# Kernel optimization log

Measured on AMD Instinct MI355X. Metric: run time of the kernel, lower is better.

The kernel has to match this reference:

```python
import jax, jax.numpy as jnp
import numpy as np

N = 50000      # num nodes
EG = 1600000   # num edges (avg degree 32)
IN = 64        # in_dim
OUT = 64       # out_dim
H = 4          # num_heads
D = OUT // H   # per-head dim


def setup_inputs() -> dict:
    key = jax.random.key(0)
    ks = jax.random.split(key, 12)
    s = 1.0 / np.sqrt(IN)
    return {
        "x": jax.random.normal(ks[0], (N, IN), jnp.float32),
        "edge_attr": jax.random.normal(ks[1], (EG, IN), jnp.float32),
        "edge_index": jax.random.randint(ks[2], (2, EG), 0, N, jnp.int32),
        "Wq": jax.random.uniform(ks[3], (OUT, IN), jnp.float32, -s, s),
        "bq": jax.random.uniform(ks[4], (OUT,), jnp.float32, -s, s),
        "Wk": jax.random.uniform(ks[5], (OUT, IN), jnp.float32, -s, s),
        "bk": jax.random.uniform(ks[6], (OUT,), jnp.float32, -s, s),
        "We": jax.random.uniform(ks[7], (OUT, IN), jnp.float32, -s, s),
        "be": jax.random.uniform(ks[8], (OUT,), jnp.float32, -s, s),
        "Wv": jax.random.uniform(ks[9], (OUT, IN), jnp.float32, -s, s),
        "bv": jax.random.uniform(ks[10], (OUT,), jnp.float32, -s, s),
    }


def reference(x, edge_attr, edge_index, Wq, bq, Wk, bk, We, be, Wv, bv):
    n = x.shape[0]
    # linear projections, reshaped to [*, H, D]
    Qh = (x @ Wq.T + bq).reshape(n, H, D)
    Kh = (x @ Wk.T + bk).reshape(n, H, D)
    Vh = (x @ Wv.T + bv).reshape(n, H, D)
    Ee = (edge_attr @ We.T + be).reshape(-1, H, D)
    src = edge_index[0]
    dst = edge_index[1]
    # per-edge score: sum_d K[src] * Q[dst] / sqrt(D) * E  -> [E, H]
    score = ((Kh[src] * Qh[dst]) * (1.0 / np.sqrt(D)) * Ee).sum(-1)
    score = jnp.exp(jnp.clip(score, -5.0, 5.0))            # [E, H]
    msg = Vh[src] * score[..., None]                        # [E, H, D]
    wV = jax.ops.segment_sum(msg, dst, num_segments=n)      # [N, H, D]
    # note: original forward returns wV without dividing by Z
    return wV.reshape(n, H * D)
```

## Files before the change

### kernel.cpp

```cpp
#include <hip/hip_runtime.h>


__global__ __launch_bounds__(256) void proj_kernel(
    const float* __restrict__ x,
    const float* __restrict__ Wq, const float* __restrict__ bq,
    const float* __restrict__ Wk, const float* __restrict__ bk,
    const float* __restrict__ Wv, const float* __restrict__ bv,
    float* __restrict__ Q, float* __restrict__ K, float* __restrict__ V,
    int n)
{
    __shared__ float WqT[64 * 65];
    __shared__ float WkT[64 * 65];
    __shared__ float WvT[64 * 65];
    __shared__ float xs[4][4][64];

    const int tid  = threadIdx.x;
    const int wave = tid >> 6;
    const int lane = tid & 63;

    #pragma unroll
    for (int k = 0; k < 16; ++k) {
        int idx = tid + k * 256;
        int j = idx >> 6, i = idx & 63;
        WqT[i * 65 + j] = Wq[idx];
        WkT[i * 65 + j] = Wk[idx];
        WvT[i * 65 + j] = Wv[idx];
    }
    const float bqv = bq[lane];
    const float bkv = bk[lane];
    const float bvv = bv[lane];
    __syncthreads();

    for (int blockbase = blockIdx.x * 16; blockbase < n;
         blockbase += gridDim.x * 16) {
        int base = blockbase + wave * 4;
        #pragma unroll
        for (int j = 0; j < 4; ++j) {
            int node = base + j;
            xs[wave][j][lane] = (node < n) ? x[node * 64 + lane] : 0.f;
        }
        __syncthreads();

        float accq[4], acck[4], accv[4];
        #pragma unroll
        for (int j = 0; j < 4; ++j) { accq[j] = bqv; acck[j] = bkv; accv[j] = bvv; }

        #pragma unroll
        for (int f = 0; f < 16; ++f) {
            float wq[4], wk[4], wv[4];
            #pragma unroll
            for (int u = 0; u < 4; ++u) {
                int i = 4 * f + u;
                wq[u] = WqT[i * 65 + lane];
                wk[u] = WkT[i * 65 + lane];
                wv[u] = WvT[i * 65 + lane];
            }
            #pragma unroll
            for (int j = 0; j < 4; ++j) {
                float4 xv = *reinterpret_cast<const float4*>(&xs[wave][j][4 * f]);
                accq[j] = fmaf(xv.x, wq[0], accq[j]);
                accq[j] = fmaf(xv.y, wq[1], accq[j]);
                accq[j] = fmaf(xv.z, wq[2], accq[j]);
                accq[j] = fmaf(xv.w, wq[3], accq[j]);
                acck[j] = fmaf(xv.x, wk[0], acck[j]);
                acck[j] = fmaf(xv.y, wk[1], acck[j]);
                acck[j] = fmaf(xv.z, wk[2], acck[j]);
                acck[j] = fmaf(xv.w, wk[3], acck[j]);
                accv[j] = fmaf(xv.x, wv[0], accv[j]);
                accv[j] = fmaf(xv.y, wv[1], accv[j]);
                accv[j] = fmaf(xv.z, wv[2], accv[j]);
                accv[j] = fmaf(xv.w, wv[3], accv[j]);
            }
        }

        #pragma unroll
        for (int j = 0; j < 4; ++j) {
            int node = base + j;
            if (node < n) {
                Q[node * 64 + lane] = accq[j];
                K[node * 64 + lane] = acck[j];
                V[node * 64 + lane] = accv[j];
            }
        }
        __syncthreads();
    }
}

__global__ __launch_bounds__(256, 4) void edge_kernel(
    const float* __restrict__ ea, const int* __restrict__ ei,
    const float* __restrict__ Q, const float* __restrict__ K,
    const float* __restrict__ V,
    const float* __restrict__ We, const float* __restrict__ be,
    float* __restrict__ out, int EG)
{
    __shared__ float eas[4][128];

    const int tid  = threadIdx.x;
    const int wave = tid >> 6;
    const int lane = tid & 63;

    float wr[64];
    {
        const float4* wrow = reinterpret_cast<const float4*>(We + (size_t)lane * 64);
        #pragma unroll
        for (int f = 0; f < 16; ++f) {
            float4 t4 = wrow[f];
            wr[4 * f + 0] = t4.x;
            wr[4 * f + 1] = t4.y;
            wr[4 * f + 2] = t4.z;
            wr[4 * f + 3] = t4.w;
        }
    }
    #pragma unroll
    for (int i = 0; i < 64; ++i)
        asm volatile("" : "+v"(wr[i]));
    const float bias = be[lane];

    const int W    = gridDim.x * 4;
    const int wid  = blockIdx.x * 4 + __builtin_amdgcn_readfirstlane(wave);
    const int step = W * 2;
    int base = wid * 2;
    if (base >= EG) return;

    int2   nsrc = *reinterpret_cast<const int2*>(&ei[base]);
    int2   ndst = *reinterpret_cast<const int2*>(&ei[EG + base]);
    float2 nea  = *reinterpret_cast<const float2*>(&ea[(size_t)base * 64 + 2 * lane]);

    for (; base < EG; base += step) {
        const int2   srcs = nsrc;
        const int2   dsts = ndst;
        const float2 eav  = nea;

        const int nb = base + step;
        if (nb < EG) {
            nsrc = *reinterpret_cast<const int2*>(&ei[nb]);
            ndst = *reinterpret_cast<const int2*>(&ei[EG + nb]);
            nea  = *reinterpret_cast<const float2*>(&ea[(size_t)nb * 64 + 2 * lane]);
        }

        *reinterpret_cast<float2*>(&eas[wave][2 * lane]) = eav;
        __builtin_amdgcn_wave_barrier();

        const bool has1 = (base + 1) < EG;
        float kv0 = K[(size_t)srcs.x * 64 + lane];
        float qv0 = Q[(size_t)dsts.x * 64 + lane];
        float vv0 = V[(size_t)srcs.x * 64 + lane];
        float kv1 = 0.f, qv1 = 0.f, vv1 = 0.f;
        if (has1) {
            kv1 = K[(size_t)srcs.y * 64 + lane];
            qv1 = Q[(size_t)dsts.y * 64 + lane];
            vv1 = V[(size_t)srcs.y * 64 + lane];
        }

        float acc0 = bias, acc1 = bias;
        const float4* r0 = reinterpret_cast<const float4*>(&eas[wave][0]);
        const float4* r1 = reinterpret_cast<const float4*>(&eas[wave][64]);
        #pragma unroll
        for (int f = 0; f < 16; ++f) {
            float4 a0 = r0[f];
            float4 a1 = r1[f];
            acc0 = fmaf(a0.x, wr[4 * f + 0], acc0);
            acc0 = fmaf(a0.y, wr[4 * f + 1], acc0);
            acc0 = fmaf(a0.z, wr[4 * f + 2], acc0);
            acc0 = fmaf(a0.w, wr[4 * f + 3], acc0);
            acc1 = fmaf(a1.x, wr[4 * f + 0], acc1);
            acc1 = fmaf(a1.y, wr[4 * f + 1], acc1);
            acc1 = fmaf(a1.z, wr[4 * f + 2], acc1);
            acc1 = fmaf(a1.w, wr[4 * f + 3], acc1);
        }

        {
            float t = kv0 * qv0 * 0.25f * acc0;
            t += __shfl_xor(t, 1);
            t += __shfl_xor(t, 2);
            t += __shfl_xor(t, 4);
            t += __shfl_xor(t, 8);
            t = fminf(fmaxf(t, -5.f), 5.f);
            float s = __expf(t);
            atomicAdd(&out[(size_t)dsts.x * 64 + lane], vv0 * s);
        }
        if (has1) {
            float t = kv1 * qv1 * 0.25f * acc1;
            t += __shfl_xor(t, 1);
            t += __shfl_xor(t, 2);
            t += __shfl_xor(t, 4);
            t += __shfl_xor(t, 8);
            t = fminf(fmaxf(t, -5.f), 5.f);
            float s = __expf(t);
            atomicAdd(&out[(size_t)dsts.y * 64 + lane], vv1 * s);
        }
        __builtin_amdgcn_wave_barrier();
    }
}

extern "C" void kernel_launch(void* const* d_in, const int* in_sizes, int n_in,
                              void* d_out, int out_size, void* d_ws, size_t ws_size,
                              hipStream_t stream) {
    const float* x   = (const float*)d_in[0];
    const float* ea  = (const float*)d_in[1];
    const int*   ei  = (const int*)d_in[2];
    const float* Wq  = (const float*)d_in[3];
    const float* bq  = (const float*)d_in[4];
    const float* Wk  = (const float*)d_in[5];
    const float* bk  = (const float*)d_in[6];
    const float* We  = (const float*)d_in[7];
    const float* be  = (const float*)d_in[8];
    const float* Wv  = (const float*)d_in[9];
    const float* bv  = (const float*)d_in[10];
    float* out = (float*)d_out;

    const int n  = in_sizes[0] / 64;
    const int EG = in_sizes[1] / 64;

    float* Q = (float*)d_ws;
    float* K = Q + (size_t)n * 64;
    float* V = K + (size_t)n * 64;

    hipMemsetAsync(d_out, 0, (size_t)out_size * sizeof(float), stream);

    const int projGrid = (n + 15) / 16;
    proj_kernel<<<projGrid, 256, 0, stream>>>(x, Wq, bq, Wk, bk, Wv, bv,
                                              Q, K, V, n);

    const int edgeGrid = 4096;
    edge_kernel<<<edgeGrid, 256, 0, stream>>>(ea, ei, Q, K, V, We, be,
                                              out, EG);
}
```

Before: 485.4 us.

## Interleave K/V per node and software-pipeline gathers one iteration ahead

The projection now writes K and V interleaved per node, so each source node's K and V rows sit contiguously in one 512-byte block. The edge loop becomes a two-stage prefetch: edge indices are loaded two iterations ahead, and the edge-attribute, K, V and Q gathers one iteration ahead, so gather latency overlaps the We matvec and the atomics. The cost is more live registers in a kernel that already holds 64 weight registers under a 4-blocks-per-CU launch bound, which could cause spills or lower occupancy.

```diff
diff --git a/kernel.cpp b/kernel.cpp
--- a/kernel.cpp
+++ b/kernel.cpp
@@ -6,7 +6,7 @@
     const float* __restrict__ Wq, const float* __restrict__ bq,
     const float* __restrict__ Wk, const float* __restrict__ bk,
     const float* __restrict__ Wv, const float* __restrict__ bv,
-    float* __restrict__ Q, float* __restrict__ K, float* __restrict__ V,
+    float* __restrict__ Qb, float* __restrict__ KV,
     int n)
 {
     __shared__ float WqT[64 * 65];
@@ -77,9 +77,9 @@
         for (int j = 0; j < 4; ++j) {
             int node = base + j;
             if (node < n) {
-                Q[node * 64 + lane] = accq[j];
-                K[node * 64 + lane] = acck[j];
-                V[node * 64 + lane] = accv[j];
+                Qb[(size_t)node * 64 + lane]       = accq[j];
+                KV[(size_t)node * 128 + lane]      = acck[j];
+                KV[(size_t)node * 128 + 64 + lane] = accv[j];
             }
         }
         __syncthreads();
@@ -88,8 +88,7 @@
 
 __global__ __launch_bounds__(256, 4) void edge_kernel(
     const float* __restrict__ ea, const int* __restrict__ ei,
-    const float* __restrict__ Q, const float* __restrict__ K,
-    const float* __restrict__ V,
+    const float* __restrict__ Qb, const float* __restrict__ KV,
     const float* __restrict__ We, const float* __restrict__ be,
     float* __restrict__ out, int EG)
 {
@@ -116,40 +115,54 @@
         asm volatile("" : "+v"(wr[i]));
     const float bias = be[lane];
 
-    const int W    = gridDim.x * 4;
+    const int nw   = gridDim.x * 4;
     const int wid  = blockIdx.x * 4 + __builtin_amdgcn_readfirstlane(wave);
-    const int step = W * 2;
+    const int step = nw * 2;
+
     int base = wid * 2;
     if (base >= EG) return;
 
-    int2   nsrc = *reinterpret_cast<const int2*>(&ei[base]);
-    int2   ndst = *reinterpret_cast<const int2*>(&ei[EG + base]);
-    float2 nea  = *reinterpret_cast<const float2*>(&ea[(size_t)base * 64 + 2 * lane]);
+    int2   sc  = *reinterpret_cast<const int2*>(&ei[base]);
+    int2   dc  = *reinterpret_cast<const int2*>(&ei[EG + base]);
+    float2 eac = *reinterpret_cast<const float2*>(&ea[(size_t)base * 64 + 2 * lane]);
+    float kv0 = KV[(size_t)sc.x * 128 + lane];
+    float vv0 = KV[(size_t)sc.x * 128 + 64 + lane];
+    float qv0 = Qb[(size_t)sc.x * 0 + (size_t)dc.x * 64 + lane];
+    float kv1 = 0.f, vv1 = 0.f, qv1 = 0.f;
+    if (base + 1 < EG) {
+        kv1 = KV[(size_t)sc.y * 128 + lane];
+        vv1 = KV[(size_t)sc.y * 128 + 64 + lane];
+        qv1 = Qb[(size_t)dc.y * 64 + lane];
+    }
+    int2 sn = sc, dn = dc;
+    if (base + step < EG) {
+        sn = *reinterpret_cast<const int2*>(&ei[base + step]);
+        dn = *reinterpret_cast<const int2*>(&ei[EG + base + step]);
+    }
 
     for (; base < EG; base += step) {
-        const int2   srcs = nsrc;
-        const int2   dsts = ndst;
-        const float2 eav  = nea;
-
-        const int nb = base + step;
-        if (nb < EG) {
-            nsrc = *reinterpret_cast<const int2*>(&ei[nb]);
-            ndst = *reinterpret_cast<const int2*>(&ei[EG + nb]);
-            nea  = *reinterpret_cast<const float2*>(&ea[(size_t)nb * 64 + 2 * lane]);
-        }
-
-        *reinterpret_cast<float2*>(&eas[wave][2 * lane]) = eav;
+        *reinterpret_cast<float2*>(&eas[wave][2 * lane]) = eac;
         __builtin_amdgcn_wave_barrier();
 
-        const bool has1 = (base + 1) < EG;
-        float kv0 = K[(size_t)srcs.x * 64 + lane];
-        float qv0 = Q[(size_t)dsts.x * 64 + lane];
-        float vv0 = V[(size_t)srcs.x * 64 + lane];
-        float kv1 = 0.f, qv1 = 0.f, vv1 = 0.f;
-        if (has1) {
-            kv1 = K[(size_t)srcs.y * 64 + lane];
-            qv1 = Q[(size_t)dsts.y * 64 + lane];
-            vv1 = V[(size_t)srcs.y * 64 + lane];
+        const int nb1 = base + step;
+        const int nb2 = base + 2 * step;
+
+        int2 snn = sn, dnn = dn;
+        if (nb2 < EG) {
+            snn = *reinterpret_cast<const int2*>(&ei[nb2]);
+            dnn = *reinterpret_cast<const int2*>(&ei[EG + nb2]);
+        }
+        float2 ean  = make_float2(0.f, 0.f);
+        float kv0n = 0.f, vv0n = 0.f, qv0n = 0.f;
+        float kv1n = 0.f, vv1n = 0.f, qv1n = 0.f;
+        if (nb1 < EG) {
+            ean  = *reinterpret_cast<const float2*>(&ea[(size_t)nb1 * 64 + 2 * lane]);
+            kv0n = KV[(size_t)sn.x * 128 + lane];
+            vv0n = KV[(size_t)sn.x * 128 + 64 + lane];
+            qv0n = Qb[(size_t)dn.x * 64 + lane];
+            kv1n = KV[(size_t)sn.y * 128 + lane];
+            vv1n = KV[(size_t)sn.y * 128 + 64 + lane];
+            qv1n = Qb[(size_t)dn.y * 64 + lane];
         }
 
         float acc0 = bias, acc1 = bias;
@@ -177,9 +190,9 @@
             t += __shfl_xor(t, 8);
             t = fminf(fmaxf(t, -5.f), 5.f);
             float s = __expf(t);
-            atomicAdd(&out[(size_t)dsts.x * 64 + lane], vv0 * s);
-        }
-        if (has1) {
+            atomicAdd(&out[(size_t)dc.x * 64 + lane], vv0 * s);
+        }
+        if (base + 1 < EG) {
             float t = kv1 * qv1 * 0.25f * acc1;
             t += __shfl_xor(t, 1);
             t += __shfl_xor(t, 2);
@@ -187,9 +200,14 @@
             t += __shfl_xor(t, 8);
             t = fminf(fmaxf(t, -5.f), 5.f);
             float s = __expf(t);
-            atomicAdd(&out[(size_t)dsts.y * 64 + lane], vv1 * s);
+            atomicAdd(&out[(size_t)dc.y * 64 + lane], vv1 * s);
         }
         __builtin_amdgcn_wave_barrier();
+
+        sc = sn;  dc = dn;  sn = snn;  dn = dnn;
+        eac = ean;
+        kv0 = kv0n; vv0 = vv0n; qv0 = qv0n;
+        kv1 = kv1n; vv1 = vv1n; qv1 = qv1n;
     }
 }
 
@@ -212,17 +230,16 @@
     const int n  = in_sizes[0] / 64;
     const int EG = in_sizes[1] / 64;
 
-    float* Q = (float*)d_ws;
-    float* K = Q + (size_t)n * 64;
-    float* V = K + (size_t)n * 64;
+    float* Qb = (float*)d_ws;
+    float* KV = Qb + (size_t)n * 64;
 
     hipMemsetAsync(d_out, 0, (size_t)out_size * sizeof(float), stream);
 
     const int projGrid = (n + 15) / 16;
     proj_kernel<<<projGrid, 256, 0, stream>>>(x, Wq, bq, Wk, bk, Wv, bv,
-                                              Q, K, V, n);
+                                              Qb, KV, n);
 
     const int edgeGrid = 4096;
-    edge_kernel<<<edgeGrid, 256, 0, stream>>>(ea, ei, Q, K, V, We, be,
+    edge_kernel<<<edgeGrid, 256, 0, stream>>>(ea, ei, Qb, KV, We, be,
                                               out, EG);
 }
```

After: 568.0 us. 1.17x slower.
